# Performance work log

Measured on AMD Instinct MI355X. Metric: run time of the kernel, lower is better.

The kernel has to match this reference:

```python
import jax, jax.numpy as jnp
import numpy as np

B, L, H = 32, 512, 1024
Q = 128
VA_H = 256

def setup_inputs() -> dict:
    key = jax.random.key(0)
    ks = jax.random.split(key, 12)
    hidden_states = jax.random.normal(ks[0], (B, L, H), dtype=jnp.float32)
    # Build valid inclusive spans: start in [2, L-16), length in [0, 8)
    asp_s = jax.random.randint(ks[1], (B, Q), 2, L - 16)
    asp_e = asp_s + jax.random.randint(ks[2], (B, Q), 0, 8)
    opi_s = jax.random.randint(ks[3], (B, Q), 2, L - 16)
    opi_e = opi_s + jax.random.randint(ks[4], (B, Q), 0, 8)
    null = jax.random.uniform(ks[5], (B, Q)) < 0.1
    asp_s = jnp.where(null, 0, asp_s)
    quad_spans = jnp.stack([asp_s, asp_e, opi_s, opi_e], axis=-1).astype(jnp.int64)
    quad_mask = (jax.random.uniform(ks[6], (B, Q)) > 0.3).astype(jnp.float32)
    # MLP params (torch Linear: y = x @ W.T + b), kaiming-ish scale
    def lin(k, out_d, in_d):
        return jax.random.normal(k, (out_d, in_d), dtype=jnp.float32) / np.sqrt(in_d)
    W1 = lin(ks[7], VA_H, 3 * H); b1 = jnp.zeros((VA_H,), jnp.float32)
    W2 = lin(ks[8], VA_H // 2, VA_H); b2 = jnp.zeros((VA_H // 2,), jnp.float32)
    W3 = lin(ks[9], 2, VA_H // 2); b3 = jnp.zeros((2,), jnp.float32)
    return {"hidden_states": hidden_states, "quad_spans": quad_spans,
            "quad_mask": quad_mask, "W1": W1, "b1": b1, "W2": W2, "b2": b2,
            "W3": W3, "b3": b3}

def _pool_spans(hidden_states, s, e):
    # hidden_states: [B,L,H]; s,e: [B,Q] inclusive indices
    pos = jnp.arange(hidden_states.shape[1])  # [L]
    valid = (s >= 2) & (e >= s)               # [B,Q]
    m = (pos[None, None, :] >= s[..., None]) & (pos[None, None, :] <= e[..., None])
    m = (m & valid[..., None]).astype(hidden_states.dtype)  # [B,Q,L]
    cnt = jnp.maximum(m.sum(-1, keepdims=True), 1.0)        # [B,Q,1]
    mean = jnp.einsum('bql,blh->bqh', m, hidden_states) / cnt
    sep = hidden_states[:, 1:2, :]                           # [B,1,H] fallback
    return jnp.where(valid[..., None], mean, sep)

def reference(hidden_states, quad_spans, quad_mask, W1, b1, W2, b2, W3, b3):
    h_asp = _pool_spans(hidden_states, quad_spans[..., 0], quad_spans[..., 1])
    h_opi = _pool_spans(hidden_states, quad_spans[..., 2], quad_spans[..., 3])
    h_pair = jnp.concatenate([h_asp, h_opi, h_asp * h_opi], axis=-1)  # [B,Q,3H]
    x = jax.nn.gelu(h_pair @ W1.T + b1, approximate=False)  # torch GELU = erf
    x = jax.nn.gelu(x @ W2.T + b2, approximate=False)
    va = jax.nn.sigmoid(x @ W3.T + b3) * 8.0 + 1.0          # [B,Q,2] in [1,9]
    # Invalid pairs stay zero, matching the torch loop's skipped entries
    return va * (quad_mask >= 0.5).astype(va.dtype)[..., None]
```

## Files before the change

### kernel.cpp

```cpp
#include <hip/hip_runtime.h>
#include <hip/hip_bf16.h>
#include <math.h>

typedef __bf16 bf16x8 __attribute__((ext_vector_type(8)));
typedef float f32x4 __attribute__((ext_vector_type(4)));

__device__ __forceinline__ unsigned short f2bf(float x) {
    union { float f; unsigned int u; } v; v.f = x;
    unsigned int r = v.u + 0x7fffu + ((v.u >> 16) & 1u);
    return (unsigned short)(r >> 16);
}
__device__ __forceinline__ float gelu_exact(float v) {
    return 0.5f * v * (1.0f + erff(v * 0.70710678118654752f));
}

__global__ __launch_bounds__(256) void prep_kernel(const float* __restrict__ hs,
                                                   const int* __restrict__ spans,
                                                   const float* __restrict__ W1,
                                                   unsigned short* __restrict__ hp,
                                                   unsigned short* __restrict__ w1b) {
    const int blk = blockIdx.x;
    const int tid = threadIdx.x;

    if (blk >= 4096) {
        const int i = (blk - 4096) * 256 + tid;
        float4 f = ((const float4*)W1)[i];
        ushort4 u;
        u.x = f2bf(f.x); u.y = f2bf(f.y); u.z = f2bf(f.z); u.w = f2bf(f.w);
        ((ushort4*)w1b)[i] = u;
        return;
    }

    const int pair = blk;
    const int b = pair >> 7;

    const bool is64 = (spans[1] == 0);
    int s_a, e_a, s_o, e_o;
    if (is64) {
        s_a = spans[(pair * 4 + 0) * 2]; e_a = spans[(pair * 4 + 1) * 2];
        s_o = spans[(pair * 4 + 2) * 2]; e_o = spans[(pair * 4 + 3) * 2];
    } else {
        s_a = spans[pair * 4 + 0]; e_a = spans[pair * 4 + 1];
        s_o = spans[pair * 4 + 2]; e_o = spans[pair * 4 + 3];
    }

    const float4* base = (const float4*)hs + (size_t)b * 512 * 256;

    float4 A, O;
    if (s_a >= 2 && e_a >= s_a) {
        float sx = 0.f, sy = 0.f, sz = 0.f, sw = 0.f;
        for (int t = s_a; t <= e_a; ++t) {
            float4 v = base[t * 256 + tid];
            sx += v.x; sy += v.y; sz += v.z; sw += v.w;
        }
        float inv = 1.0f / (float)(e_a - s_a + 1);
        A.x = sx * inv; A.y = sy * inv; A.z = sz * inv; A.w = sw * inv;
    } else {
        A = base[256 + tid];
    }
    if (s_o >= 2 && e_o >= s_o) {
        float sx = 0.f, sy = 0.f, sz = 0.f, sw = 0.f;
        for (int t = s_o; t <= e_o; ++t) {
            float4 v = base[t * 256 + tid];
            sx += v.x; sy += v.y; sz += v.z; sw += v.w;
        }
        float inv = 1.0f / (float)(e_o - s_o + 1);
        O.x = sx * inv; O.y = sy * inv; O.z = sz * inv; O.w = sw * inv;
    } else {
        O = base[256 + tid];
    }

    unsigned short* row = hp + (size_t)pair * 3072;
    const int d = tid * 4;
    ushort4 pa, po, pp;
    pa.x = f2bf(A.x); pa.y = f2bf(A.y); pa.z = f2bf(A.z); pa.w = f2bf(A.w);
    po.x = f2bf(O.x); po.y = f2bf(O.y); po.z = f2bf(O.z); po.w = f2bf(O.w);
    pp.x = f2bf(A.x * O.x); pp.y = f2bf(A.y * O.y);
    pp.z = f2bf(A.z * O.z); pp.w = f2bf(A.w * O.w);
    *(ushort4*)(row + d) = pa;
    *(ushort4*)(row + 1024 + d) = po;
    *(ushort4*)(row + 2048 + d) = pp;
}

__global__ __launch_bounds__(256, 8) void gemm1_gelu(const unsigned short* __restrict__ A,
                                                     const unsigned short* __restrict__ Bw,
                                                     const float* __restrict__ b1,
                                                     unsigned short* __restrict__ x1) {
    __shared__ __align__(16) unsigned short As[2][16 * 64];
    __shared__ __align__(16) unsigned short Bs[2][64 * 64];

    const int tid = threadIdx.x;
    const int lane = tid & 63;
    const int wid = tid >> 6;
    const int quad = lane >> 4;
    const int l16 = lane & 15;
    const int m0 = blockIdx.x * 16;
    const int n0 = blockIdx.y * 64;

    const int srow = tid >> 3;
    const int lch = (tid & 7) ^ (srow & 7);
    const unsigned short* Aptr = A + (size_t)(m0 + srow) * 3072 + lch * 8;
    const unsigned short* Bptr = Bw + (size_t)(n0 + srow) * 3072 + lch * 8;

    int aoff[2], boff[2];
#pragma unroll
    for (int h = 0; h < 2; ++h) {
        int pc = (h * 4 + quad) ^ (l16 & 7);
        aoff[h] = l16 * 64 + pc * 8;
        const int brow = wid * 16 + l16;
        pc = (h * 4 + quad) ^ (brow & 7);
        boff[h] = brow * 64 + pc * 8;
    }

    f32x4 acc = {};

    if (tid < 128)
        __builtin_amdgcn_global_load_lds(
            (const __attribute__((address_space(1))) void*)Aptr,
            (__attribute__((address_space(3))) void*)(&As[0][tid * 8]), 16, 0, 0);
#pragma unroll
    for (int j = 0; j < 2; ++j)
        __builtin_amdgcn_global_load_lds(
            (const __attribute__((address_space(1))) void*)(Bptr + (size_t)j * 32 * 3072),
            (__attribute__((address_space(3))) void*)(&Bs[0][(j * 256 + tid) * 8]), 16, 0, 0);

    for (int it = 0; it < 48; ++it) {
        const int cur = it & 1;
        __syncthreads();
        if (it + 1 < 48) {
            const int nxt = cur ^ 1;
            const int kadv = (it + 1) * 64;
            if (tid < 128)
                __builtin_amdgcn_global_load_lds(
                    (const __attribute__((address_space(1))) void*)(Aptr + kadv),
                    (__attribute__((address_space(3))) void*)(&As[nxt][tid * 8]), 16, 0, 0);
#pragma unroll
            for (int j = 0; j < 2; ++j)
                __builtin_amdgcn_global_load_lds(
                    (const __attribute__((address_space(1))) void*)(Bptr + (size_t)j * 32 * 3072 + kadv),
                    (__attribute__((address_space(3))) void*)(&Bs[nxt][(j * 256 + tid) * 8]), 16, 0, 0);
        }
#pragma unroll
        for (int h = 0; h < 2; ++h) {
            bf16x8 a = *(const bf16x8*)&As[cur][aoff[h]];
            bf16x8 b = *(const bf16x8*)&Bs[cur][boff[h]];
            acc = __builtin_amdgcn_mfma_f32_16x16x32_bf16(a, b, acc, 0, 0, 0);
        }
    }

    const int n = n0 + wid * 16 + l16;
    const float bn = b1[n];
#pragma unroll
    for (int rr = 0; rr < 4; ++rr) {
        const int m = m0 + quad * 4 + rr;
        x1[(size_t)m * 256 + n] = f2bf(gelu_exact(acc[rr] + bn));
    }
}

__global__ __launch_bounds__(256) void mlp2_head(const unsigned short* __restrict__ x1,
                                                 const float* __restrict__ W2f,
                                                 const float* __restrict__ b2,
                                                 const float* __restrict__ W3,
                                                 const float* __restrict__ b3,
                                                 const float* __restrict__ mask,
                                                 float* __restrict__ out) {
    __shared__ __align__(16) unsigned short Xs[32][72];
    __shared__ __align__(16) unsigned short Ws[128][72];
    __shared__ float X2[32][132];

    const int tid = threadIdx.x;
    const int lane = tid & 63;
    const int wid = tid >> 6;
    const int wM = (wid >> 1) * 16;
    const int wN = (wid & 1) * 64;
    const int quad = lane >> 4;
    const int l16 = lane & 15;
    const int m0 = blockIdx.x * 32;

    f32x4 acc[4] = {};

    for (int k0 = 0; k0 < 256; k0 += 64) {
        {
            const int r = tid >> 3, c = (tid & 7) * 8;
            *(uint4*)&Xs[r][c] = *(const uint4*)(x1 + (size_t)(m0 + r) * 256 + k0 + c);
        }
#pragma unroll
        for (int p = 0; p < 4; ++p) {
            const int v = tid + p * 256;
            const int r = v >> 3, c = (v & 7) * 8;
            const float* src = W2f + (size_t)r * 256 + k0 + c;
            float4 f0 = *(const float4*)src;
            float4 f1 = *(const float4*)(src + 4);
            ushort4 u;
            u.x = f2bf(f0.x); u.y = f2bf(f0.y); u.z = f2bf(f0.z); u.w = f2bf(f0.w);
            *(ushort4*)&Ws[r][c] = u;
            u.x = f2bf(f1.x); u.y = f2bf(f1.y); u.z = f2bf(f1.z); u.w = f2bf(f1.w);
            *(ushort4*)&Ws[r][c + 4] = u;
        }
        __syncthreads();
#pragma unroll
        for (int kk = 0; kk < 64; kk += 32) {
            bf16x8 a = *(const bf16x8*)&Xs[wM + l16][kk + quad * 8];
#pragma unroll
            for (int ni = 0; ni < 4; ++ni) {
                bf16x8 b = *(const bf16x8*)&Ws[wN + ni * 16 + l16][kk + quad * 8];
                acc[ni] = __builtin_amdgcn_mfma_f32_16x16x32_bf16(a, b, acc[ni], 0, 0, 0);
            }
        }
        __syncthreads();
    }

#pragma unroll
    for (int ni = 0; ni < 4; ++ni) {
        const int n = wN + ni * 16 + l16;
        const float bn = b2[n];
#pragma unroll
        for (int rr = 0; rr < 4; ++rr) {
            const int m = wM + quad * 4 + rr;
            X2[m][n] = gelu_exact(acc[ni][rr] + bn);
        }
    }
    __syncthreads();

    const int p = tid >> 3;
    const int cc = (tid & 7) * 16;
    float a0 = 0.f, a1 = 0.f;
#pragma unroll
    for (int j = 0; j < 16; ++j) {
        const float xv = X2[p][cc + j];
        a0 += xv * W3[cc + j];
        a1 += xv * W3[128 + cc + j];
    }
    a0 += __shfl_xor(a0, 1); a0 += __shfl_xor(a0, 2); a0 += __shfl_xor(a0, 4);
    a1 += __shfl_xor(a1, 1); a1 += __shfl_xor(a1, 2); a1 += __shfl_xor(a1, 4);
    if ((tid & 7) == 0) {
        const int pair = m0 + p;
        const float mk = (mask[pair] >= 0.5f) ? 1.0f : 0.0f;
        out[pair * 2 + 0] = ((1.0f / (1.0f + expf(-(a0 + b3[0])))) * 8.0f + 1.0f) * mk;
        out[pair * 2 + 1] = ((1.0f / (1.0f + expf(-(a1 + b3[1])))) * 8.0f + 1.0f) * mk;
    }
}

extern "C" void kernel_launch(void* const* d_in, const int* in_sizes, int n_in,
                              void* d_out, int out_size, void* d_ws, size_t ws_size,
                              hipStream_t stream) {
    const float* hs   = (const float*)d_in[0];
    const int*   spans= (const int*)d_in[1];
    const float* mask = (const float*)d_in[2];
    const float* W1   = (const float*)d_in[3];
    const float* b1   = (const float*)d_in[4];
    const float* W2   = (const float*)d_in[5];
    const float* b2   = (const float*)d_in[6];
    const float* W3   = (const float*)d_in[7];
    const float* b3   = (const float*)d_in[8];
    float* out = (float*)d_out;

    unsigned short* hp  = (unsigned short*)d_ws;
    unsigned short* w1b = (unsigned short*)((char*)d_ws + 25165824);
    unsigned short* x1  = (unsigned short*)((char*)d_ws + 26738688);

    prep_kernel<<<dim3(4864), dim3(256), 0, stream>>>(hs, spans, W1, hp, w1b);
    gemm1_gelu<<<dim3(256, 4), dim3(256), 0, stream>>>(hp, w1b, b1, x1);
    mlp2_head<<<dim3(128), dim3(256), 0, stream>>>(x1, W2, b2, W3, b3, mask, out);
}
```

Baseline: 157.2 us.

## Enlarge GEMM1 tiles to 32x64x128 and pre-convert W2 to bf16 in prep

The first GEMM now computes a 32-row by 64-column tile per block with a 128-wide K step, so each wave runs two MFMA accumulators and every B fragment is reused across both row halves. This halves the grid and the number of K iterations, which cuts redundant W1 tile loads and barrier overhead. Occupancy drops (launch bounds 8 to 2) and shared memory per block grows. Separately, W2 is converted to bf16 once in the prep kernel, so the head kernel no longer converts it to bf16 in every block.

```diff
diff --git a/kernel.cpp b/kernel.cpp
--- a/kernel.cpp
+++ b/kernel.cpp
@@ -17,17 +17,27 @@
 __global__ __launch_bounds__(256) void prep_kernel(const float* __restrict__ hs,
                                                    const int* __restrict__ spans,
                                                    const float* __restrict__ W1,
+                                                   const float* __restrict__ W2,
                                                    unsigned short* __restrict__ hp,
-                                                   unsigned short* __restrict__ w1b) {
+                                                   unsigned short* __restrict__ w1b,
+                                                   unsigned short* __restrict__ w2b) {
     const int blk = blockIdx.x;
     const int tid = threadIdx.x;
 
     if (blk >= 4096) {
-        const int i = (blk - 4096) * 256 + tid;
-        float4 f = ((const float4*)W1)[i];
-        ushort4 u;
-        u.x = f2bf(f.x); u.y = f2bf(f.y); u.z = f2bf(f.z); u.w = f2bf(f.w);
-        ((ushort4*)w1b)[i] = u;
+        if (blk < 4864) {
+            const int i = (blk - 4096) * 256 + tid;
+            float4 f = ((const float4*)W1)[i];
+            ushort4 u;
+            u.x = f2bf(f.x); u.y = f2bf(f.y); u.z = f2bf(f.z); u.w = f2bf(f.w);
+            ((ushort4*)w1b)[i] = u;
+        } else {
+            const int i = (blk - 4864) * 256 + tid;
+            float4 f = ((const float4*)W2)[i];
+            ushort4 u;
+            u.x = f2bf(f.x); u.y = f2bf(f.y); u.z = f2bf(f.z); u.w = f2bf(f.w);
+            ((ushort4*)w2b)[i] = u;
+        }
         return;
     }
 
@@ -82,83 +92,108 @@
     *(ushort4*)(row + 2048 + d) = pp;
 }
 
-__global__ __launch_bounds__(256, 8) void gemm1_gelu(const unsigned short* __restrict__ A,
+__global__ __launch_bounds__(256, 2) void gemm1_gelu(const unsigned short* __restrict__ A,
                                                      const unsigned short* __restrict__ Bw,
                                                      const float* __restrict__ b1,
                                                      unsigned short* __restrict__ x1) {
-    __shared__ __align__(16) unsigned short As[2][16 * 64];
-    __shared__ __align__(16) unsigned short Bs[2][64 * 64];
+    __shared__ __align__(16) unsigned short As[2][32 * 128];
+    __shared__ __align__(16) unsigned short Bs[2][64 * 128];
 
     const int tid = threadIdx.x;
     const int lane = tid & 63;
     const int wid = tid >> 6;
     const int quad = lane >> 4;
     const int l16 = lane & 15;
-    const int m0 = blockIdx.x * 16;
+    const int m0 = blockIdx.x * 32;
     const int n0 = blockIdx.y * 64;
 
-    const int srow = tid >> 3;
-    const int lch = (tid & 7) ^ (srow & 7);
-    const unsigned short* Aptr = A + (size_t)(m0 + srow) * 3072 + lch * 8;
-    const unsigned short* Bptr = Bw + (size_t)(n0 + srow) * 3072 + lch * 8;
-
-    int aoff[2], boff[2];
-#pragma unroll
-    for (int h = 0; h < 2; ++h) {
-        int pc = (h * 4 + quad) ^ (l16 & 7);
-        aoff[h] = l16 * 64 + pc * 8;
+    const int arow = tid >> 4;
+    const int ac = tid & 15;
+    const unsigned short* Aptr[2];
+#pragma unroll
+    for (int p = 0; p < 2; ++p) {
+        const int row = arow + p * 16;
+        const int lch = ((ac & 7) ^ (row & 7)) | (ac & 8);
+        Aptr[p] = A + (size_t)(m0 + row) * 3072 + lch * 8;
+    }
+    const unsigned short* Bptr[4];
+#pragma unroll
+    for (int p = 0; p < 4; ++p) {
+        const int row = arow + p * 16;
+        const int lch = ((ac & 7) ^ (row & 7)) | (ac & 8);
+        Bptr[p] = Bw + (size_t)(n0 + row) * 3072 + lch * 8;
+    }
+
+    int aoff[2][4], boff[4];
+#pragma unroll
+    for (int h = 0; h < 4; ++h) {
+        const int c = h * 4 + quad;
+#pragma unroll
+        for (int mh = 0; mh < 2; ++mh) {
+            const int row = mh * 16 + l16;
+            const int pc = ((c & 7) ^ (row & 7)) | (c & 8);
+            aoff[mh][h] = row * 128 + pc * 8;
+        }
         const int brow = wid * 16 + l16;
-        pc = (h * 4 + quad) ^ (brow & 7);
-        boff[h] = brow * 64 + pc * 8;
-    }
-
-    f32x4 acc = {};
-
-    if (tid < 128)
+        const int pcb = ((c & 7) ^ (brow & 7)) | (c & 8);
+        boff[h] = brow * 128 + pcb * 8;
+    }
+
+    f32x4 acc[2] = {};
+
+#pragma unroll
+    for (int p = 0; p < 2; ++p)
         __builtin_amdgcn_global_load_lds(
-            (const __attribute__((address_space(1))) void*)Aptr,
-            (__attribute__((address_space(3))) void*)(&As[0][tid * 8]), 16, 0, 0);
-#pragma unroll
-    for (int j = 0; j < 2; ++j)
+            (const __attribute__((address_space(1))) void*)Aptr[p],
+            (__attribute__((address_space(3))) void*)(&As[0][(p * 256 + tid) * 8]), 16, 0, 0);
+#pragma unroll
+    for (int p = 0; p < 4; ++p)
         __builtin_amdgcn_global_load_lds(
-            (const __attribute__((address_space(1))) void*)(Bptr + (size_t)j * 32 * 3072),
-            (__attribute__((address_space(3))) void*)(&Bs[0][(j * 256 + tid) * 8]), 16, 0, 0);
-
-    for (int it = 0; it < 48; ++it) {
+            (const __attribute__((address_space(1))) void*)Bptr[p],
+            (__attribute__((address_space(3))) void*)(&Bs[0][(p * 256 + tid) * 8]), 16, 0, 0);
+
+    for (int it = 0; it < 24; ++it) {
         const int cur = it & 1;
         __syncthreads();
-        if (it + 1 < 48) {
+        if (it + 1 < 24) {
             const int nxt = cur ^ 1;
-            const int kadv = (it + 1) * 64;
-            if (tid < 128)
+            const int kadv = (it + 1) * 128;
+#pragma unroll
+            for (int p = 0; p < 2; ++p)
                 __builtin_amdgcn_global_load_lds(
-                    (const __attribute__((address_space(1))) void*)(Aptr + kadv),
-                    (__attribute__((address_space(3))) void*)(&As[nxt][tid * 8]), 16, 0, 0);
-#pragma unroll
-            for (int j = 0; j < 2; ++j)
+                    (const __attribute__((address_space(1))) void*)(Aptr[p] + kadv),
+                    (__attribute__((address_space(3))) void*)(&As[nxt][(p * 256 + tid) * 8]), 16, 0, 0);
+#pragma unroll
+            for (int p = 0; p < 4; ++p)
                 __builtin_amdgcn_global_load_lds(
-                    (const __attribute__((address_space(1))) void*)(Bptr + (size_t)j * 32 * 3072 + kadv),
-                    (__attribute__((address_space(3))) void*)(&Bs[nxt][(j * 256 + tid) * 8]), 16, 0, 0);
-        }
-#pragma unroll
-        for (int h = 0; h < 2; ++h) {
-            bf16x8 a = *(const bf16x8*)&As[cur][aoff[h]];
+                    (const __attribute__((address_space(1))) void*)(Bptr[p] + kadv),
+                    (__attribute__((address_space(3))) void*)(&Bs[nxt][(p * 256 + tid) * 8]), 16, 0, 0);
+        }
+#pragma unroll
+        for (int h = 0; h < 4; ++h) {
             bf16x8 b = *(const bf16x8*)&Bs[cur][boff[h]];
-            acc = __builtin_amdgcn_mfma_f32_16x16x32_bf16(a, b, acc, 0, 0, 0);
+#pragma unroll
+            for (int mh = 0; mh < 2; ++mh) {
+                bf16x8 a = *(const bf16x8*)&As[cur][aoff[mh][h]];
+                acc[mh] = __builtin_amdgcn_mfma_f32_16x16x32_bf16(a, b, acc[mh], 0, 0, 0);
+            }
         }
     }
 
     const int n = n0 + wid * 16 + l16;
     const float bn = b1[n];
 #pragma unroll
-    for (int rr = 0; rr < 4; ++rr) {
-        const int m = m0 + quad * 4 + rr;
-        x1[(size_t)m * 256 + n] = f2bf(gelu_exact(acc[rr] + bn));
+    for (int mh = 0; mh < 2; ++mh) {
+#pragma unroll
+        for (int rr = 0; rr < 4; ++rr) {
+            const int m = m0 + mh * 16 + quad * 4 + rr;
+            x1[(size_t)m * 256 + n] = f2bf(gelu_exact(acc[mh][rr] + bn));
+        }
     }
 }
 
 __global__ __launch_bounds__(256) void mlp2_head(const unsigned short* __restrict__ x1,
-                                                 const float* __restrict__ W2f,
+                                                 const unsigned short* __restrict__ w2b,
                                                  const float* __restrict__ b2,
                                                  const float* __restrict__ W3,
                                                  const float* __restrict__ b3,
@@ -188,14 +223,7 @@
         for (int p = 0; p < 4; ++p) {
             const int v = tid + p * 256;
             const int r = v >> 3, c = (v & 7) * 8;
-            const float* src = W2f + (size_t)r * 256 + k0 + c;
-            float4 f0 = *(const float4*)src;
-            float4 f1 = *(const float4*)(src + 4);
-            ushort4 u;
-            u.x = f2bf(f0.x); u.y = f2bf(f0.y); u.z = f2bf(f0.z); u.w = f2bf(f0.w);
-            *(ushort4*)&Ws[r][c] = u;
-            u.x = f2bf(f1.x); u.y = f2bf(f1.y); u.z = f2bf(f1.z); u.w = f2bf(f1.w);
-            *(ushort4*)&Ws[r][c + 4] = u;
+            *(uint4*)&Ws[r][c] = *(const uint4*)(w2b + (size_t)r * 256 + k0 + c);
         }
         __syncthreads();
 #pragma unroll
@@ -258,8 +286,9 @@
     unsigned short* hp  = (unsigned short*)d_ws;
     unsigned short* w1b = (unsigned short*)((char*)d_ws + 25165824);
     unsigned short* x1  = (unsigned short*)((char*)d_ws + 26738688);
-
-    prep_kernel<<<dim3(4864), dim3(256), 0, stream>>>(hs, spans, W1, hp, w1b);
-    gemm1_gelu<<<dim3(256, 4), dim3(256), 0, stream>>>(hp, w1b, b1, x1);
-    mlp2_head<<<dim3(128), dim3(256), 0, stream>>>(x1, W2, b2, W3, b3, mask, out);
-}
+    unsigned short* w2b = (unsigned short*)((char*)d_ws + 28835840);
+
+    prep_kernel<<<dim3(4896), dim3(256), 0, stream>>>(hs, spans, W1, W2, hp, w1b, w2b);
+    gemm1_gelu<<<dim3(128, 4), dim3(256), 0, stream>>>(hp, w1b, b1, x1);
+    mlp2_head<<<dim3(128), dim3(256), 0, stream>>>(x1, w2b, b2, W3, b3, mask, out);
+}
```

Result: faster. 148.7 us (-5.4%).
